# Performance work log

Measured on AMD Instinct MI355X. Metric: run time of the kernel, lower is better.

## Reference

```python
import jax, jax.numpy as jnp
import numpy as np

EPS = 1e-5  # BatchNorm1d default eps


def _xavier_uniform(key, shape):
    # torch xavier: fan_in = shape[1]*prod(shape[2:]), fan_out = shape[0]*prod(shape[2:])
    rf = int(np.prod(shape[2:])) if len(shape) > 2 else 1
    fan_in = shape[1] * rf
    fan_out = shape[0] * rf
    bound = float(np.sqrt(6.0 / (fan_in + fan_out)))
    return jax.random.uniform(key, shape, jnp.float32, -bound, bound)


def setup_inputs() -> dict:
    key = jax.random.key(0)
    ks = jax.random.split(key, 6)
    d_in, h1, h2, d_out = 256, 512, 512, 256
    B = 4096
    x = jax.random.normal(ks[0], (B, 1, d_in), dtype=jnp.float32)
    W1 = _xavier_uniform(ks[1], (h1, d_in))
    b1 = jnp.zeros((h1,), jnp.float32)
    gamma = jnp.ones((1, 1, 1), jnp.float32)   # BatchNorm1d(1) weight
    beta = jnp.zeros((1, 1, 1), jnp.float32)   # BatchNorm1d(1) bias
    coeffs2 = _xavier_uniform(ks[2], (2, h2, h1, 16))
    bias2 = jnp.zeros((1, h2), jnp.float32)
    coeffs3 = _xavier_uniform(ks[3], (2, d_out, h2, 8))
    bias3 = jnp.zeros((1, d_out), jnp.float32)
    return {"x": x, "W1": W1, "b1": b1, "gamma": gamma, "beta": beta,
            "coeffs2": coeffs2, "bias2": bias2, "coeffs3": coeffs3, "bias3": bias3}


def _fourier_kan(x, coeffs, bias, gridsize):
    # x: (N, in)  coeffs: (2, out, in, grid)  ->  (N, out)
    k = jnp.arange(1, gridsize + 1, dtype=x.dtype)          # (grid,)
    arg = x[:, :, None] * k                                  # (N, in, grid) -- basis computed ONCE
    y = jnp.einsum('nig,oig->no', jnp.cos(arg), coeffs[0])
    y = y + jnp.einsum('nig,oig->no', jnp.sin(arg), coeffs[1])
    return y + bias


def reference(x, W1, b1, gamma, beta, coeffs2, bias2, coeffs3, bias3):
    # x: (B, 1, d_in)
    h = jnp.einsum('bcd,hd->bch', x, W1) + b1                # Linear -> (B,1,h1)
    # BatchNorm1d(1), training-mode batch stats over (N, L) for the single channel
    mean = jnp.mean(h, axis=(0, 2), keepdims=True)
    var = jnp.mean((h - mean) ** 2, axis=(0, 2), keepdims=True)
    h = gamma * (h - mean) * jax.lax.rsqrt(var + EPS) + beta
    h = jax.nn.relu(h)
    h = h.reshape(-1, h.shape[-1])                           # (B, h1)
    h = _fourier_kan(h, coeffs2, bias2, 16)                  # (B, h2)
    h = _fourier_kan(h, coeffs3, bias3, 8)                   # (B, out)
    return jax.nn.softmax(h, axis=1)
```

## Files before the change

kernel.cpp:

```cpp
#include <hip/hip_runtime.h>
#include <hip/hip_fp16.h>
#include <stdint.h>

typedef unsigned short u16;
typedef unsigned int u32;
typedef long i64;
typedef short bf16x8 __attribute__((ext_vector_type(8)));
typedef float f32x4 __attribute__((ext_vector_type(4)));

#define SCALE_C   1024.f
#define INV_SCALE 0.0009765625f

__device__ __forceinline__ float bf2f(u16 v) { return __uint_as_float(((u32)v) << 16); }

__device__ __forceinline__ u16 f2bf(float a) {
  u32 u = __float_as_uint(a); u += 0x7FFFu + ((u >> 16) & 1u); return (u16)(u >> 16);
}

__device__ __forceinline__ u32 packbf2(float a, float b) {
  u32 ua = __float_as_uint(a); ua += 0x7FFFu + ((ua >> 16) & 1u);
  u32 ub = __float_as_uint(b); ub += 0x7FFFu + ((ub >> 16) & 1u);
  return (ua >> 16) | (ub & 0xFFFF0000u);
}

__device__ __forceinline__ u32 packfp8x4(float a, float b, float c, float d) {
  u32 lo = (u32)__builtin_amdgcn_cvt_pk_fp8_f32(a, b, 0, false);
  return (u32)__builtin_amdgcn_cvt_pk_fp8_f32(c, d, (int)lo, true);
}

__device__ __forceinline__ float inval(const void* p, int idx, int isf) {
  return isf ? ((const float*)p)[idx] : bf2f(((const u16*)p)[idx]);
}

__device__ __forceinline__ void async_cp16(const void* g, void* l) {
  __builtin_amdgcn_global_load_lds(
      (const __attribute__((address_space(1))) void*)g,
      (__attribute__((address_space(3))) void*)l, 16, 0, 0);
}

__device__ __forceinline__ void split_body(
    const void* __restrict__ src, u16* __restrict__ dst, int i, int isf, int lo_pos)
{
  int row = i >> 6, g = i & 63;
  float v[4];
  if (isf) {
    float4 t = ((const float4*)src)[i];
    v[0] = t.x; v[1] = t.y; v[2] = t.z; v[3] = t.w;
  } else {
    uint2 t = ((const uint2*)src)[i];
    const u16* p = (const u16*)&t;
    v[0] = bf2f(p[0]); v[1] = bf2f(p[1]); v[2] = bf2f(p[2]); v[3] = bf2f(p[3]);
  }
  u16 hi[4]; float lo[4];
  #pragma unroll
  for (int j = 0; j < 4; ++j) { hi[j] = f2bf(v[j]); lo[j] = v[j] - bf2f(hi[j]); }
  u32 hw0 = (u32)hi[0] | ((u32)hi[1] << 16);
  u32 hw1 = (u32)hi[2] | ((u32)hi[3] << 16);
  u32 lw0 = packbf2(lo[0], lo[1]);
  u32 lw1 = packbf2(lo[2], lo[3]);
  u32* base = (u32*)(dst + (size_t)row * 768);
  int c = g * 2;
  base[c] = hw0; base[c + 1] = hw1;
  if (lo_pos == 1) {
    base[128 + c] = lw0; base[128 + c + 1] = lw1;
    base[256 + c] = hw0; base[256 + c + 1] = hw1;
  } else {
    base[128 + c] = hw0; base[128 + c + 1] = hw1;
    base[256 + c] = lw0; base[256 + c + 1] = lw1;
  }
}

__global__ __launch_bounds__(256) void prep_all_kernel(
    const void* __restrict__ x, const void* __restrict__ W1,
    u16* __restrict__ Xs, u16* __restrict__ W1s,
    const void* __restrict__ c2, unsigned char* __restrict__ w2f8,
    const void* __restrict__ c3, unsigned char* __restrict__ w3f8,
    int* __restrict__ flag)
{
  __shared__ int sf[4];
  const int t = threadIdx.x, wave = t >> 6;
  {
    float v = fabsf(bf2f(((const u16*)W1)[t & 127]));
    int bad = !(v < 1e6f);
    unsigned long long b = __ballot(bad);
    if ((t & 63) == 0) sf[wave] = (b != 0ull) ? 1 : 0;
  }
  __syncthreads();
  const int isf = sf[0] | sf[1] | sf[2] | sf[3];
  const int bid = blockIdx.x;
  if (bid == 0 && t == 0) *flag = isf;
  if (bid < 1024) {
    split_body(x, Xs, bid * 256 + t, isf, 1);
  } else if (bid < 1152) {
    split_body(W1, W1s, (bid - 1024) * 256 + t, isf, 2);
  } else if (bid < 2176) {
    int u = (bid - 1152) * 256 + t;
    int o = u >> 9, i = u & 511;
    u32* d = (u32*)(w2f8 + (size_t)o * 16384 + i * 32);
    if (isf) {
      const float4* f0 = (const float4*)((const float*)c2 + ((size_t)o * 512 + i) * 16);
      const float4* f1 = (const float4*)((const float*)c2 + (size_t)512 * 512 * 16 + ((size_t)o * 512 + i) * 16);
      #pragma unroll
      for (int j = 0; j < 4; ++j) { float4 v = f0[j]; d[j]   = packfp8x4(v.x*SCALE_C, v.y*SCALE_C, v.z*SCALE_C, v.w*SCALE_C); }
      #pragma unroll
      for (int j = 0; j < 4; ++j) { float4 v = f1[j]; d[4+j] = packfp8x4(v.x*SCALE_C, v.y*SCALE_C, v.z*SCALE_C, v.w*SCALE_C); }
    } else {
      const u16* s0 = (const u16*)c2 + ((size_t)o * 512 + i) * 16;
      const u16* s1 = (const u16*)c2 + (size_t)512 * 512 * 16 + ((size_t)o * 512 + i) * 16;
      #pragma unroll
      for (int j = 0; j < 4; ++j) d[j]   = packfp8x4(bf2f(s0[4*j])*SCALE_C, bf2f(s0[4*j+1])*SCALE_C, bf2f(s0[4*j+2])*SCALE_C, bf2f(s0[4*j+3])*SCALE_C);
      #pragma unroll
      for (int j = 0; j < 4; ++j) d[4+j] = packfp8x4(bf2f(s1[4*j])*SCALE_C, bf2f(s1[4*j+1])*SCALE_C, bf2f(s1[4*j+2])*SCALE_C, bf2f(s1[4*j+3])*SCALE_C);
    }
  } else {
    int u = (bid - 2176) * 256 + t;
    int o = u >> 9, i = u & 511;
    u32* d = (u32*)(w3f8 + (size_t)o * 8192 + i * 16);
    if (isf) {
      const float4* f0 = (const float4*)((const float*)c3 + ((size_t)o * 512 + i) * 8);
      const float4* f1 = (const float4*)((const float*)c3 + (size_t)256 * 512 * 8 + ((size_t)o * 512 + i) * 8);
      #pragma unroll
      for (int j = 0; j < 2; ++j) { float4 v = f0[j]; d[j]   = packfp8x4(v.x*SCALE_C, v.y*SCALE_C, v.z*SCALE_C, v.w*SCALE_C); }
      #pragma unroll
      for (int j = 0; j < 2; ++j) { float4 v = f1[j]; d[2+j] = packfp8x4(v.x*SCALE_C, v.y*SCALE_C, v.z*SCALE_C, v.w*SCALE_C); }
    } else {
      const u16* s0 = (const u16*)c3 + ((size_t)o * 512 + i) * 8;
      const u16* s1 = (const u16*)c3 + (size_t)256 * 512 * 8 + ((size_t)o * 512 + i) * 8;
      #pragma unroll
      for (int j = 0; j < 2; ++j) d[j]   = packfp8x4(bf2f(s0[4*j])*SCALE_C, bf2f(s0[4*j+1])*SCALE_C, bf2f(s0[4*j+2])*SCALE_C, bf2f(s0[4*j+3])*SCALE_C);
      #pragma unroll
      for (int j = 0; j < 2; ++j) d[2+j] = packfp8x4(bf2f(s1[4*j])*SCALE_C, bf2f(s1[4*j+1])*SCALE_C, bf2f(s1[4*j+2])*SCALE_C, bf2f(s1[4*j+3])*SCALE_C);
    }
  }
}

#define L1_LD 136
__global__ __launch_bounds__(256) void l1_kernel(
    const u16* __restrict__ xs, const u16* __restrict__ w1s, const void* __restrict__ b1,
    const int* __restrict__ flag, float* __restrict__ H, float2* __restrict__ PT)
{
  __shared__ u16 sA[128 * L1_LD];
  __shared__ u16 sB[64 * L1_LD];
  __shared__ float redbuf[8];
  const int n0 = blockIdx.x * 128, o0 = blockIdx.y * 64;
  const int t = threadIdx.x, wave = t >> 6, lane = t & 63, quad = lane >> 4, l16 = lane & 15;
  const int isf = *flag;
  f32x4 acc[2][4] = {};
  for (int ks = 0; ks < 768; ks += 128) {
    #pragma unroll
    for (int r = 0; r < 8; ++r) {
      int idx = t + r * 256;
      int row = idx >> 4, col = idx & 15;
      const uint4* src = (const uint4*)(xs + (size_t)(n0 + row) * 768 + ks) + col;
      *(uint4*)&sA[row * L1_LD + col * 8] = *src;
    }
    #pragma unroll
    for (int r = 0; r < 4; ++r) {
      int idx = t + r * 256;
      int row = idx >> 4, col = idx & 15;
      const uint4* src = (const uint4*)(w1s + (size_t)(o0 + row) * 768 + ks) + col;
      *(uint4*)&sB[row * L1_LD + col * 8] = *src;
    }
    __syncthreads();
    #pragma unroll
    for (int kk = 0; kk < 128; kk += 32) {
      bf16x8 bfr[4];
      #pragma unroll
      for (int fo = 0; fo < 4; ++fo)
        bfr[fo] = *(const bf16x8*)&sB[(fo * 16 + l16) * L1_LD + kk + quad * 8];
      #pragma unroll
      for (int fm = 0; fm < 2; ++fm) {
        bf16x8 av = *(const bf16x8*)&sA[(wave * 32 + fm * 16 + l16) * L1_LD + kk + quad * 8];
        #pragma unroll
        for (int fo = 0; fo < 4; ++fo)
          acc[fm][fo] = __builtin_amdgcn_mfma_f32_16x16x32_bf16(av, bfr[fo], acc[fm][fo], 0, 0, 0);
      }
    }
    __syncthreads();
  }
  float s = 0.f, sq = 0.f;
  #pragma unroll
  for (int fm = 0; fm < 2; ++fm)
  #pragma unroll
  for (int fo = 0; fo < 4; ++fo) {
    int o = o0 + fo * 16 + l16;
    float bias = inval(b1, o, isf);
    #pragma unroll
    for (int r = 0; r < 4; ++r) {
      int n = n0 + wave * 32 + fm * 16 + quad * 4 + r;
      float h = acc[fm][fo][r] + bias;
      H[(size_t)n * 512 + o] = h;
      s += h; sq += h * h;
    }
  }
  #pragma unroll
  for (int off = 32; off; off >>= 1) { s += __shfl_down(s, off); sq += __shfl_down(sq, off); }
  if (lane == 0) { redbuf[wave] = s; redbuf[4 + wave] = sq; }
  __syncthreads();
  if (t == 0) {
    float S = redbuf[0] + redbuf[1] + redbuf[2] + redbuf[3];
    float Q = redbuf[4] + redbuf[5] + redbuf[6] + redbuf[7];
    PT[blockIdx.y * 32 + blockIdx.x] = make_float2(S, Q);
  }
}

#define K2_LDB 128
template <int OT>
__global__ __launch_bounds__(256) void kan2_kernel(
    const float* __restrict__ H, const unsigned char* __restrict__ w2f8,
    const void* __restrict__ gammap, const void* __restrict__ betap,
    const int* __restrict__ flag, const float2* __restrict__ PT,
    float* __restrict__ P, int kzT)
{
  constexpr int FO = OT / 32;
  constexpr int BP = OT / 32;
  __shared__ unsigned char sA8[64 * K2_LDB];
  __shared__ unsigned char sB8[OT * K2_LDB];
  __shared__ float sred[8];
  const int n0 = blockIdx.x * 64, o0 = blockIdx.y * OT, kz = blockIdx.z;
  const int t = threadIdx.x, wave = t >> 6, lane = t & 63, quad = lane >> 4, l16 = lane & 15;
  const int wm = (wave & 1) * 32, wo = (wave >> 1) * (OT / 2);
  const int isf = *flag;
  const int am = t >> 2, ai = t & 3;
  const int q = 128 / kzT, rr = 128 % kzT;
  const int nst = q + (kz < rr ? 1 : 0);
  const int i0 = (kz * q + (kz < rr ? kz : rr)) * 4;
  const int r0 = t >> 3, seg = t & 7;
  const unsigned char* bsrc = w2f8 + (size_t)(o0 + r0) * 16384 + (size_t)i0 * 32
                              + ((seg * 16) ^ ((r0 & 7) << 4));
  const float* hsrc = H + (size_t)(n0 + am) * 512 + i0 + ai;
  unsigned char* ldsB = &sB8[wave * 8 * K2_LDB];
  #pragma unroll
  for (int p = 0; p < BP; ++p)
    async_cp16(bsrc + (size_t)p * 32 * 16384, ldsB + p * 32 * K2_LDB);
  float ph = *hsrc;
  {
    float2 pt = PT[t];
    float ss = pt.x, qs = pt.y;
    #pragma unroll
    for (int off = 32; off; off >>= 1) { ss += __shfl_down(ss, off); qs += __shfl_down(qs, off); }
    if (lane == 0) { sred[wave] = ss; sred[4 + wave] = qs; }
  }
  __syncthreads();
  const float Ssum = sred[0] + sred[1] + sred[2] + sred[3];
  const float Qsum = sred[4] + sred[5] + sred[6] + sred[7];
  const float Nn = 4096.f * 512.f;
  const float mean = Ssum / Nn;
  const float rstd = rsqrtf(Qsum / Nn - mean * mean + 1e-5f);
  const float gs = inval(gammap, 0, isf) * rstd;
  const float beta = inval(betap, 0, isf);
  const int acol0 = (ai * 32) ^ ((am & 7) << 4);
  const int acol1 = (ai * 32 + 16) ^ ((am & 7) << 4);
  const int csw   = (l16 & 7) << 4;
  f32x4 acc[2][FO] = {};
  for (int s = 0; s < nst; ++s) {
    {
      float a = fmaxf((ph - mean) * gs + beta, 0.f);
      float s1, c1; __sincosf(a, &s1, &c1);
      float t2 = c1 + c1;
      float cg[16], sg[16];
      cg[0] = c1; sg[0] = s1;
      cg[1] = fmaf(t2, c1, -1.f); sg[1] = t2 * s1;
      #pragma unroll
      for (int g = 2; g < 16; ++g) {
        cg[g] = fmaf(t2, cg[g-1], -cg[g-2]);
        sg[g] = fmaf(t2, sg[g-1], -sg[g-2]);
      }
      u32 pk[8];
      #pragma unroll
      for (int j = 0; j < 4; ++j) pk[j]   = packfp8x4(cg[4*j], cg[4*j+1], cg[4*j+2], cg[4*j+3]);
      #pragma unroll
      for (int j = 0; j < 4; ++j) pk[4+j] = packfp8x4(sg[4*j], sg[4*j+1], sg[4*j+2], sg[4*j+3]);
      *(uint4*)&sA8[am * K2_LDB + acol0] = *(uint4*)&pk[0];
      *(uint4*)&sA8[am * K2_LDB + acol1] = *(uint4*)&pk[4];
    }
    __syncthreads();
    hsrc += 4;
    if (s + 1 < nst) ph = *hsrc;
    #pragma unroll
    for (int kk = 0; kk < 128; kk += 32) {
      const int cb = (kk + quad * 8) ^ csw;
      i64 bfr[FO], afr[2];
      #pragma unroll
      for (int fo = 0; fo < FO; ++fo)
        bfr[fo] = *(const i64*)&sB8[(wo + fo * 16 + l16) * K2_LDB + cb];
      #pragma unroll
      for (int fm = 0; fm < 2; ++fm)
        afr[fm] = *(const i64*)&sA8[(wm + fm * 16 + l16) * K2_LDB + cb];
      #pragma unroll
      for (int fm = 0; fm < 2; ++fm)
      #pragma unroll
      for (int fo = 0; fo < FO; ++fo)
        acc[fm][fo] = __builtin_amdgcn_mfma_f32_16x16x32_fp8_fp8(afr[fm], bfr[fo], acc[fm][fo], 0, 0, 0);
    }
    __syncthreads();
    bsrc += 128;
    if (s + 1 < nst) {
      #pragma unroll
      for (int p = 0; p < BP; ++p)
        async_cp16(bsrc + (size_t)p * 32 * 16384, ldsB + p * 32 * K2_LDB);
    }
  }
  float* Pk = P + (size_t)kz * (4096 * 512);
  #pragma unroll
  for (int fm = 0; fm < 2; ++fm)
  #pragma unroll
  for (int fo = 0; fo < FO; ++fo) {
    int o = o0 + wo + fo * 16 + l16;
    #pragma unroll
    for (int r = 0; r < 4; ++r) {
      int n = n0 + wm + fm * 16 + quad * 4 + r;
      Pk[(size_t)n * 512 + o] = acc[fm][fo][r] * INV_SCALE;
    }
  }
}

#define K3_LDB 128
__global__ __launch_bounds__(256) void kan3_kernel(
    const float* __restrict__ P2, const void* __restrict__ bias2,
    const unsigned char* __restrict__ w3f8,
    const int* __restrict__ flag, float* __restrict__ Q, int kzT2)
{
  __shared__ unsigned char sA8[32 * K3_LDB];
  __shared__ unsigned char sB8[256 * K3_LDB];
  const int n0 = blockIdx.x * 32, kz = blockIdx.z;
  const int t = threadIdx.x, wave = t >> 6, lane = t & 63, quad = lane >> 4, l16 = lane & 15;
  const int wo = wave * 64;
  const int am = t >> 3, ai = t & 7;
  const int nst = 10 + (kz < 4 ? 1 : 0);
  const int i0 = (kz * 10 + (kz < 4 ? kz : 4)) * 8;
  const int r0 = t >> 3, seg = t & 7;
  const int isf = *flag;
  const unsigned char* bsrc = w3f8 + (size_t)r0 * 8192 + (size_t)i0 * 16
                              + ((seg * 16) ^ ((r0 & 7) << 4));
  const float* psrc = P2 + (size_t)(n0 + am) * 512 + i0 + ai;
  unsigned char* ldsB = &sB8[wave * 8 * K3_LDB];
  const int acol = (ai * 16) ^ ((am & 7) << 4);
  const int csw  = (l16 & 7) << 4;
  f32x4 acc[2][4] = {};
  #pragma unroll
  for (int p = 0; p < 8; ++p)
    async_cp16(bsrc + (size_t)p * 32 * 8192, ldsB + p * 32 * K3_LDB);
  float ph;
  {
    float v = inval(bias2, i0 + ai, isf);
    for (int k = 0; k < kzT2; ++k) v += psrc[(size_t)k * 4096 * 512];
    ph = v;
  }
  for (int s = 0; s < nst; ++s) {
    {
      float s1, c1; __sincosf(ph, &s1, &c1);
      float t2 = c1 + c1;
      float cg[8], sg[8];
      cg[0] = c1; sg[0] = s1;
      cg[1] = fmaf(t2, c1, -1.f); sg[1] = t2 * s1;
      #pragma unroll
      for (int g = 2; g < 8; ++g) {
        cg[g] = fmaf(t2, cg[g-1], -cg[g-2]);
        sg[g] = fmaf(t2, sg[g-1], -sg[g-2]);
      }
      u32 pk[4];
      pk[0] = packfp8x4(cg[0], cg[1], cg[2], cg[3]);
      pk[1] = packfp8x4(cg[4], cg[5], cg[6], cg[7]);
      pk[2] = packfp8x4(sg[0], sg[1], sg[2], sg[3]);
      pk[3] = packfp8x4(sg[4], sg[5], sg[6], sg[7]);
      *(uint4*)&sA8[am * K3_LDB + acol] = *(uint4*)&pk[0];
    }
    __syncthreads();
    psrc += 8;
    if (s + 1 < nst) {
      float v = inval(bias2, i0 + (s + 1) * 8 + ai, isf);
      for (int k = 0; k < kzT2; ++k) v += psrc[(size_t)k * 4096 * 512];
      ph = v;
    }
    #pragma unroll
    for (int kk = 0; kk < 128; kk += 32) {
      const int cb = (kk + quad * 8) ^ csw;
      i64 bfr[4], afr[2];
      #pragma unroll
      for (int fo = 0; fo < 4; ++fo)
        bfr[fo] = *(const i64*)&sB8[(wo + fo * 16 + l16) * K3_LDB + cb];
      #pragma unroll
      for (int fm = 0; fm < 2; ++fm)
        afr[fm] = *(const i64*)&sA8[(fm * 16 + l16) * K3_LDB + cb];
      #pragma unroll
      for (int fm = 0; fm < 2; ++fm)
      #pragma unroll
      for (int fo = 0; fo < 4; ++fo)
        acc[fm][fo] = __builtin_amdgcn_mfma_f32_16x16x32_fp8_fp8(afr[fm], bfr[fo], acc[fm][fo], 0, 0, 0);
    }
    __syncthreads();
    bsrc += 128;
    if (s + 1 < nst) {
      #pragma unroll
      for (int p = 0; p < 8; ++p)
        async_cp16(bsrc + (size_t)p * 32 * 8192, ldsB + p * 32 * K3_LDB);
    }
  }
  float* Qk = Q + (size_t)kz * (4096 * 256);
  #pragma unroll
  for (int fm = 0; fm < 2; ++fm)
  #pragma unroll
  for (int fo = 0; fo < 4; ++fo) {
    int o = wo + fo * 16 + l16;
    #pragma unroll
    for (int r = 0; r < 4; ++r) {
      int n = n0 + fm * 16 + quad * 4 + r;
      Qk[(size_t)n * 256 + o] = acc[fm][fo][r] * INV_SCALE;
    }
  }
}

__global__ __launch_bounds__(256) void softmax_kernel(
    const float* __restrict__ Q, const void* __restrict__ bias3,
    const int* __restrict__ flag, float* __restrict__ out)
{
  const int t = threadIdx.x, wave = t >> 6, lane = t & 63;
  const int row = blockIdx.x * 4 + wave;
  const int isf = *flag;
  size_t base = (size_t)row * 256 + lane * 4;
  float v0 = 0.f, v1 = 0.f, v2 = 0.f, v3 = 0.f;
  #pragma unroll
  for (int k = 0; k < 6; ++k) {
    float4 a = *(const float4*)(Q + (size_t)k * 4096 * 256 + base);
    v0 += a.x; v1 += a.y; v2 += a.z; v3 += a.w;
  }
  int o = lane * 4;
  v0 += inval(bias3, o + 0, isf);
  v1 += inval(bias3, o + 1, isf);
  v2 += inval(bias3, o + 2, isf);
  v3 += inval(bias3, o + 3, isf);
  float m = fmaxf(fmaxf(v0, v1), fmaxf(v2, v3));
  #pragma unroll
  for (int off = 32; off; off >>= 1) m = fmaxf(m, __shfl_xor(m, off));
  float e0 = __expf(v0 - m), e1 = __expf(v1 - m), e2 = __expf(v2 - m), e3 = __expf(v3 - m);
  float s = e0 + e1 + e2 + e3;
  #pragma unroll
  for (int off = 32; off; off >>= 1) s += __shfl_xor(s, off);
  float inv = 1.f / s;
  *(float4*)(out + base) = make_float4(e0 * inv, e1 * inv, e2 * inv, e3 * inv);
}

extern "C" void kernel_launch(void* const* d_in, const int* in_sizes, int n_in,
                              void* d_out, int out_size, void* d_ws, size_t ws_size,
                              hipStream_t stream)
{
  const void* x     = d_in[0];
  const void* W1    = d_in[1];
  const void* b1    = d_in[2];
  const void* gamma = d_in[3];
  const void* beta  = d_in[4];
  const void* c2    = d_in[5];
  const void* bias2 = d_in[6];
  const void* c3    = d_in[7];
  const void* bias3 = d_in[8];

  const bool wide2 = (ws_size >= (83ull << 20));
  const int kz2 = wide2 ? 6 : ((ws_size >= (75ull << 20)) ? 5 : 3);

  char* ws = (char*)d_ws;
  float*          H    = (float*)(ws + 0);
  unsigned char*  W2F8 = (unsigned char*)(ws + (16ull << 20));
  unsigned char*  W3F8 = (unsigned char*)(ws + (24ull << 20));
  u16*            Xs   = (u16*)(ws + (26ull << 20));
  u16*            W1s  = (u16*)(ws + (33ull << 20));
  float*          P2   = (float*)(ws + (34ull << 20));
  float*          Q3   = (float*)(ws + 0);
  size_t tail = (34ull << 20) + (size_t)kz2 * (8ull << 20) + 524288;
  float2* PT   = (float2*)(ws + tail);
  int*    FLAG = (int*)   (ws + tail + 65536);

  prep_all_kernel<<<dim3(2688), dim3(256), 0, stream>>>(x, W1, Xs, W1s, c2, W2F8, c3, W3F8, FLAG);
  l1_kernel   <<<dim3(32, 8), dim3(256), 0, stream>>>(Xs, W1s, b1, FLAG, H, PT);
  if (wide2)
    kan2_kernel<256><<<dim3(64, 2, kz2), dim3(256), 0, stream>>>(H, W2F8, gamma, beta, FLAG, PT, P2, kz2);
  else
    kan2_kernel<128><<<dim3(64, 4, kz2), dim3(256), 0, stream>>>(H, W2F8, gamma, beta, FLAG, PT, P2, kz2);
  kan3_kernel <<<dim3(128, 1, 6), dim3(256), 0, stream>>>(P2, bias2, W3F8, FLAG, Q3, kz2);
  softmax_kernel<<<dim3(1024), dim3(256), 0, stream>>>(Q3, bias3, FLAG, (float*)d_out);
}
```

Before: 211.5 us.

## Double-buffer KAN2 LDS tiles and halve L1 row tile, fixing split-K at 3

The KAN layer-2 kernel now double-buffers both the fp8 basis tile and the weight tile in LDS. The next stage's async weight copy and its sin/cos basis computation are issued before the current stage's MFMA loop, so each stage needs one barrier instead of two. The layer-1 GEMM tile drops from 128 to 64 rows, doubling the block count, and the partial-stat reduction now reads 512 entries. The OT=256 variant and the workspace-dependent split-K choice are removed and kz fixed at 3, which may lose parallelism when a larger workspace is available.

New measurement: 214.2 us. Within noise of the previous version (+1.3%).

```diff
diff --git a/kernel.cpp b/kernel.cpp
--- a/kernel.cpp
+++ b/kernel.cpp
@@ -36,6 +36,23 @@
   __builtin_amdgcn_global_load_lds(
       (const __attribute__((address_space(1))) void*)g,
       (__attribute__((address_space(3))) void*)l, 16, 0, 0);
+}
+
+__device__ __forceinline__ void basis16(float a, u32* pk) {
+  float s1, c1; __sincosf(a, &s1, &c1);
+  float t2 = c1 + c1;
+  float cg[16], sg[16];
+  cg[0] = c1; sg[0] = s1;
+  cg[1] = fmaf(t2, c1, -1.f); sg[1] = t2 * s1;
+  #pragma unroll
+  for (int g = 2; g < 16; ++g) {
+    cg[g] = fmaf(t2, cg[g-1], -cg[g-2]);
+    sg[g] = fmaf(t2, sg[g-1], -sg[g-2]);
+  }
+  #pragma unroll
+  for (int j = 0; j < 4; ++j) pk[j]   = packfp8x4(cg[4*j], cg[4*j+1], cg[4*j+2], cg[4*j+3]);
+  #pragma unroll
+  for (int j = 0; j < 4; ++j) pk[4+j] = packfp8x4(sg[4*j], sg[4*j+1], sg[4*j+2], sg[4*j+3]);
 }
 
 __device__ __forceinline__ void split_body(
@@ -139,56 +156,47 @@
     const u16* __restrict__ xs, const u16* __restrict__ w1s, const void* __restrict__ b1,
     const int* __restrict__ flag, float* __restrict__ H, float2* __restrict__ PT)
 {
-  __shared__ u16 sA[128 * L1_LD];
+  __shared__ u16 sA[64 * L1_LD];
   __shared__ u16 sB[64 * L1_LD];
   __shared__ float redbuf[8];
-  const int n0 = blockIdx.x * 128, o0 = blockIdx.y * 64;
+  const int n0 = blockIdx.x * 64, o0 = blockIdx.y * 64;
   const int t = threadIdx.x, wave = t >> 6, lane = t & 63, quad = lane >> 4, l16 = lane & 15;
   const int isf = *flag;
-  f32x4 acc[2][4] = {};
+  f32x4 acc[4] = {};
   for (int ks = 0; ks < 768; ks += 128) {
     #pragma unroll
-    for (int r = 0; r < 8; ++r) {
-      int idx = t + r * 256;
-      int row = idx >> 4, col = idx & 15;
-      const uint4* src = (const uint4*)(xs + (size_t)(n0 + row) * 768 + ks) + col;
-      *(uint4*)&sA[row * L1_LD + col * 8] = *src;
-    }
-    #pragma unroll
     for (int r = 0; r < 4; ++r) {
-      int idx = t + r * 256;
-      int row = idx >> 4, col = idx & 15;
-      const uint4* src = (const uint4*)(w1s + (size_t)(o0 + row) * 768 + ks) + col;
-      *(uint4*)&sB[row * L1_LD + col * 8] = *src;
+      int idx = t + r * 256, row = idx >> 4, col = idx & 15;
+      *(uint4*)&sA[row * L1_LD + col * 8] =
+          *((const uint4*)(xs + (size_t)(n0 + row) * 768 + ks) + col);
+    }
+    #pragma unroll
+    for (int r = 0; r < 4; ++r) {
+      int idx = t + r * 256, row = idx >> 4, col = idx & 15;
+      *(uint4*)&sB[row * L1_LD + col * 8] =
+          *((const uint4*)(w1s + (size_t)(o0 + row) * 768 + ks) + col);
     }
     __syncthreads();
     #pragma unroll
     for (int kk = 0; kk < 128; kk += 32) {
-      bf16x8 bfr[4];
-      #pragma unroll
-      for (int fo = 0; fo < 4; ++fo)
-        bfr[fo] = *(const bf16x8*)&sB[(fo * 16 + l16) * L1_LD + kk + quad * 8];
-      #pragma unroll
-      for (int fm = 0; fm < 2; ++fm) {
-        bf16x8 av = *(const bf16x8*)&sA[(wave * 32 + fm * 16 + l16) * L1_LD + kk + quad * 8];
-        #pragma unroll
-        for (int fo = 0; fo < 4; ++fo)
-          acc[fm][fo] = __builtin_amdgcn_mfma_f32_16x16x32_bf16(av, bfr[fo], acc[fm][fo], 0, 0, 0);
+      bf16x8 av = *(const bf16x8*)&sA[(wave * 16 + l16) * L1_LD + kk + quad * 8];
+      #pragma unroll
+      for (int fo = 0; fo < 4; ++fo) {
+        bf16x8 bv = *(const bf16x8*)&sB[(fo * 16 + l16) * L1_LD + kk + quad * 8];
+        acc[fo] = __builtin_amdgcn_mfma_f32_16x16x32_bf16(av, bv, acc[fo], 0, 0, 0);
       }
     }
     __syncthreads();
   }
   float s = 0.f, sq = 0.f;
-  #pragma unroll
-  for (int fm = 0; fm < 2; ++fm)
   #pragma unroll
   for (int fo = 0; fo < 4; ++fo) {
     int o = o0 + fo * 16 + l16;
     float bias = inval(b1, o, isf);
     #pragma unroll
     for (int r = 0; r < 4; ++r) {
-      int n = n0 + wave * 32 + fm * 16 + quad * 4 + r;
-      float h = acc[fm][fo][r] + bias;
+      int n = n0 + wave * 16 + quad * 4 + r;
+      float h = acc[fo][r] + bias;
       H[(size_t)n * 512 + o] = h;
       s += h; sq += h * h;
     }
@@ -200,26 +208,23 @@
   if (t == 0) {
     float S = redbuf[0] + redbuf[1] + redbuf[2] + redbuf[3];
     float Q = redbuf[4] + redbuf[5] + redbuf[6] + redbuf[7];
-    PT[blockIdx.y * 32 + blockIdx.x] = make_float2(S, Q);
+    PT[blockIdx.y * 64 + blockIdx.x] = make_float2(S, Q);
   }
 }
 
 #define K2_LDB 128
-template <int OT>
 __global__ __launch_bounds__(256) void kan2_kernel(
     const float* __restrict__ H, const unsigned char* __restrict__ w2f8,
     const void* __restrict__ gammap, const void* __restrict__ betap,
     const int* __restrict__ flag, const float2* __restrict__ PT,
     float* __restrict__ P, int kzT)
 {
-  constexpr int FO = OT / 32;
-  constexpr int BP = OT / 32;
-  __shared__ unsigned char sA8[64 * K2_LDB];
-  __shared__ unsigned char sB8[OT * K2_LDB];
+  __shared__ unsigned char sA8[2][64 * K2_LDB];
+  __shared__ unsigned char sB8[2][128 * K2_LDB];
   __shared__ float sred[8];
-  const int n0 = blockIdx.x * 64, o0 = blockIdx.y * OT, kz = blockIdx.z;
+  const int n0 = blockIdx.x * 64, o0 = blockIdx.y * 128, kz = blockIdx.z;
   const int t = threadIdx.x, wave = t >> 6, lane = t & 63, quad = lane >> 4, l16 = lane & 15;
-  const int wm = (wave & 1) * 32, wo = (wave >> 1) * (OT / 2);
+  const int wm = (wave & 1) * 32, wo = (wave >> 1) * 64;
   const int isf = *flag;
   const int am = t >> 2, ai = t & 3;
   const int q = 128 / kzT, rr = 128 % kzT;
@@ -229,14 +234,15 @@
   const unsigned char* bsrc = w2f8 + (size_t)(o0 + r0) * 16384 + (size_t)i0 * 32
                               + ((seg * 16) ^ ((r0 & 7) << 4));
   const float* hsrc = H + (size_t)(n0 + am) * 512 + i0 + ai;
-  unsigned char* ldsB = &sB8[wave * 8 * K2_LDB];
-  #pragma unroll
-  for (int p = 0; p < BP; ++p)
-    async_cp16(bsrc + (size_t)p * 32 * 16384, ldsB + p * 32 * K2_LDB);
-  float ph = *hsrc;
+  const int ldsOff = wave * 8 * K2_LDB;
+  #pragma unroll
+  for (int p = 0; p < 4; ++p)
+    async_cp16(bsrc + (size_t)p * 32 * 16384, &sB8[0][ldsOff + p * 32 * K2_LDB]);
+  bsrc += 128;
+  float ph = *hsrc; hsrc += 4;
   {
-    float2 pt = PT[t];
-    float ss = pt.x, qs = pt.y;
+    float2 pa = PT[t], pb = PT[t + 256];
+    float ss = pa.x + pb.x, qs = pa.y + pb.y;
     #pragma unroll
     for (int off = 32; off; off >>= 1) { ss += __shfl_down(ss, off); qs += __shfl_down(qs, off); }
     if (lane == 0) { sred[wave] = ss; sred[4 + wave] = qs; }
@@ -251,61 +257,57 @@
   const float beta = inval(betap, 0, isf);
   const int acol0 = (ai * 32) ^ ((am & 7) << 4);
   const int acol1 = (ai * 32 + 16) ^ ((am & 7) << 4);
-  const int csw   = (l16 & 7) << 4;
-  f32x4 acc[2][FO] = {};
+  const int csw = (l16 & 7) << 4;
+  f32x4 acc[2][4] = {};
+  u32 pk[8];
+  {
+    float a = fmaxf((ph - mean) * gs + beta, 0.f);
+    basis16(a, pk);
+  }
+  if (nst > 1) { ph = *hsrc; hsrc += 4; }
+  *(uint4*)&sA8[0][am * K2_LDB + acol0] = *(uint4*)&pk[0];
+  *(uint4*)&sA8[0][am * K2_LDB + acol1] = *(uint4*)&pk[4];
+  __syncthreads();
+  int cur = 0;
   for (int s = 0; s < nst; ++s) {
-    {
+    const int nxt = cur ^ 1;
+    if (s + 1 < nst) {
+      #pragma unroll
+      for (int p = 0; p < 4; ++p)
+        async_cp16(bsrc + (size_t)p * 32 * 16384, &sB8[nxt][ldsOff + p * 32 * K2_LDB]);
+      bsrc += 128;
       float a = fmaxf((ph - mean) * gs + beta, 0.f);
-      float s1, c1; __sincosf(a, &s1, &c1);
-      float t2 = c1 + c1;
-      float cg[16], sg[16];
-      cg[0] = c1; sg[0] = s1;
-      cg[1] = fmaf(t2, c1, -1.f); sg[1] = t2 * s1;
-      #pragma unroll
-      for (int g = 2; g < 16; ++g) {
-        cg[g] = fmaf(t2, cg[g-1], -cg[g-2]);
-        sg[g] = fmaf(t2, sg[g-1], -sg[g-2]);
-      }
-      u32 pk[8];
-      #pragma unroll
-      for (int j = 0; j < 4; ++j) pk[j]   = packfp8x4(cg[4*j], cg[4*j+1], cg[4*j+2], cg[4*j+3]);
-      #pragma unroll
-      for (int j = 0; j < 4; ++j) pk[4+j] = packfp8x4(sg[4*j], sg[4*j+1], sg[4*j+2], sg[4*j+3]);
-      *(uint4*)&sA8[am * K2_LDB + acol0] = *(uint4*)&pk[0];
-      *(uint4*)&sA8[am * K2_LDB + acol1] = *(uint4*)&pk[4];
-    }
-    __syncthreads();
-    hsrc += 4;
-    if (s + 1 < nst) ph = *hsrc;
+      basis16(a, pk);
+      if (s + 2 < nst) { ph = *hsrc; hsrc += 4; }
+    }
     #pragma unroll
     for (int kk = 0; kk < 128; kk += 32) {
       const int cb = (kk + quad * 8) ^ csw;
-      i64 bfr[FO], afr[2];
-      #pragma unroll
-      for (int fo = 0; fo < FO; ++fo)
-        bfr[fo] = *(const i64*)&sB8[(wo + fo * 16 + l16) * K2_LDB + cb];
+      i64 bfr[4], afr[2];
+      #pragma unroll
+      for (int fo = 0; fo < 4; ++fo)
+        bfr[fo] = *(const i64*)&sB8[cur][(wo + fo * 16 + l16) * K2_LDB + cb];
       #pragma unroll
       for (int fm = 0; fm < 2; ++fm)
-        afr[fm] = *(const i64*)&sA8[(wm + fm * 16 + l16) * K2_LDB + cb];
+        afr[fm] = *(const i64*)&sA8[cur][(wm + fm * 16 + l16) * K2_LDB + cb];
       #pragma unroll
       for (int fm = 0; fm < 2; ++fm)
       #pragma unroll
-      for (int fo = 0; fo < FO; ++fo)
+      for (int fo = 0; fo < 4; ++fo)
         acc[fm][fo] = __builtin_amdgcn_mfma_f32_16x16x32_fp8_fp8(afr[fm], bfr[fo], acc[fm][fo], 0, 0, 0);
     }
+    if (s + 1 < nst) {
+      *(uint4*)&sA8[nxt][am * K2_LDB + acol0] = *(uint4*)&pk[0];
+      *(uint4*)&sA8[nxt][am * K2_LDB + acol1] = *(uint4*)&pk[4];
+    }
     __syncthreads();
-    bsrc += 128;
-    if (s + 1 < nst) {
-      #pragma unroll
-      for (int p = 0; p < BP; ++p)
-        async_cp16(bsrc + (size_t)p * 32 * 16384, ldsB + p * 32 * K2_LDB);
-    }
+    cur = nxt;
   }
   float* Pk = P + (size_t)kz * (4096 * 512);
   #pragma unroll
   for (int fm = 0; fm < 2; ++fm)
   #pragma unroll
-  for (int fo = 0; fo < FO; ++fo) {
+  for (int fo = 0; fo < 4; ++fo) {
     int o = o0 + wo + fo * 16 + l16;
     #pragma unroll
     for (int r = 0; r < 4; ++r) {
@@ -455,8 +457,7 @@
   const void* c3    = d_in[7];
   const void* bias3 = d_in[8];
 
-  const bool wide2 = (ws_size >= (83ull << 20));
-  const int kz2 = wide2 ? 6 : ((ws_size >= (75ull << 20)) ? 5 : 3);
+  const int kz2 = 3;
 
   char* ws = (char*)d_ws;
   float*          H    = (float*)(ws + 0);
@@ -471,11 +472,8 @@
   int*    FLAG = (int*)   (ws + tail + 65536);
 
   prep_all_kernel<<<dim3(2688), dim3(256), 0, stream>>>(x, W1, Xs, W1s, c2, W2F8, c3, W3F8, FLAG);
-  l1_kernel   <<<dim3(32, 8), dim3(256), 0, stream>>>(Xs, W1s, b1, FLAG, H, PT);
-  if (wide2)
-    kan2_kernel<256><<<dim3(64, 2, kz2), dim3(256), 0, stream>>>(H, W2F8, gamma, beta, FLAG, PT, P2, kz2);
-  else
-    kan2_kernel<128><<<dim3(64, 4, kz2), dim3(256), 0, stream>>>(H, W2F8, gamma, beta, FLAG, PT, P2, kz2);
+  l1_kernel   <<<dim3(64, 8), dim3(256), 0, stream>>>(Xs, W1s, b1, FLAG, H, PT);
+  kan2_kernel <<<dim3(64, 4, kz2), dim3(256), 0, stream>>>(H, W2F8, gamma, beta, FLAG, PT, P2, kz2);
   kan3_kernel <<<dim3(128, 1, 6), dim3(256), 0, stream>>>(P2, bias2, W3F8, FLAG, Q3, kz2);
   softmax_kernel<<<dim3(1024), dim3(256), 0, stream>>>(Q3, bias3, FLAG, (float*)d_out);
 }
```
